# Kernel tuning notes

Hardware: AMD Instinct MI355X
Metric: run time of the kernel (lower is better)

The kernel has to match this reference:

```python
import jax, jax.numpy as jnp
import numpy as np

N, E = 50000, 800000
D_IN, D_H, D_OUT = 128, 128, 64


def _gcn_conv(h, src, dst, norm, b, n):
    # h already linearly transformed: aggregate norm-weighted messages to dst
    msg = h[src] * norm[:, None]                      # [E+N, d]
    out = jax.ops.segment_sum(msg, dst, num_segments=n)
    return out + b


def setup_inputs() -> dict:
    key = jax.random.key(0)
    ks = jax.random.split(key, 5)
    x = jax.random.normal(ks[0], (N, D_IN), jnp.float32)
    edge_index = jax.random.randint(ks[1], (2, E), 0, N, jnp.int32)
    s1 = 1.0 / np.sqrt(D_IN)
    s2 = 1.0 / np.sqrt(D_H)
    W1 = jax.random.uniform(ks[2], (D_IN, D_H), jnp.float32, -s1, s1)
    b1 = jnp.zeros((D_H,), jnp.float32)
    W2 = jax.random.uniform(ks[3], (D_H, D_OUT), jnp.float32, -s2, s2)
    b2 = jnp.zeros((D_OUT,), jnp.float32)
    return {"x": x, "edge_index": edge_index, "W1": W1, "b1": b1, "W2": W2, "b2": b2}


def reference(x, edge_index, W1, b1, W2, b2):
    n = x.shape[0]
    loops = jnp.arange(n, dtype=edge_index.dtype)
    src = jnp.concatenate([edge_index[0], loops])     # add self-loops
    dst = jnp.concatenate([edge_index[1], loops])
    # symmetric normalization D^{-1/2} (A+I) D^{-1/2}; deg is in-degree incl. self-loop
    deg = jax.ops.segment_sum(jnp.ones(dst.shape[0], x.dtype), dst, num_segments=n)
    dinv = jnp.where(deg > 0, jax.lax.rsqrt(deg), 0.0)
    norm = dinv[src] * dinv[dst]
    h = _gcn_conv(x @ W1, src, dst, norm, b1, n)
    h = jax.nn.relu(h)                                # dropout = identity (eval)
    out = _gcn_conv(h @ W2, src, dst, norm, b2, n)
    return out
```

## Files before the change

kernel.cpp:

```cpp
#include <hip/hip_runtime.h>

typedef __bf16 bf16x8 __attribute__((ext_vector_type(8)));
typedef __bf16 bf16x4 __attribute__((ext_vector_type(4)));
typedef float  f32x4  __attribute__((ext_vector_type(4)));
typedef unsigned long long u64;

constexpr int PAD       = 64;
constexpr int BIN_SHIFT = 9;
constexpr int CAP       = 12288;
constexpr int SUBS      = 4;
constexpr int NPS       = 128;
constexpr int STR       = 68;
constexpr int CUR_STR   = 16;
constexpr int EPB       = 2048;


__global__ void init_k(int* __restrict__ bincur, __bf16* __restrict__ h1zero,
                       __bf16* __restrict__ h3zero) {
  int t = threadIdx.x;
  for (int i = t; i < 128 * CUR_STR; i += 256) bincur[i] = 0;
  if (t < 128) h1zero[t] = (__bf16)0.f;
  if (t < 64)  h3zero[t] = (__bf16)0.f;
}


__global__ __launch_bounds__(256) void bin_fill_k(
    const int* __restrict__ src, const int* __restrict__ dst,
    int* __restrict__ bincur, u64* __restrict__ bin_data, int E, int n) {
  __shared__ u64 pairs[EPB];
  __shared__ int binof[EPB];
  __shared__ int hist[128], cur[128], sbase[128], gbase[128];

  const int t = threadIdx.x;
  const int NB = (n + ((1 << BIN_SHIFT) - 1)) >> BIN_SHIFT;

  if (t < 128) { hist[t] = 0; cur[t] = 0; }
  __syncthreads();

  int base_e = blockIdx.x * EPB + t * 8;
  int m = E - base_e;
  m = m < 0 ? 0 : (m > 8 ? 8 : m);

  int sa[8], da[8], ba[8];
  if (m == 8) {
    int4 s0 = *reinterpret_cast<const int4*>(src + base_e);
    int4 s1 = *reinterpret_cast<const int4*>(src + base_e + 4);
    int4 d0 = *reinterpret_cast<const int4*>(dst + base_e);
    int4 d1 = *reinterpret_cast<const int4*>(dst + base_e + 4);
    sa[0]=s0.x; sa[1]=s0.y; sa[2]=s0.z; sa[3]=s0.w;
    sa[4]=s1.x; sa[5]=s1.y; sa[6]=s1.z; sa[7]=s1.w;
    da[0]=d0.x; da[1]=d0.y; da[2]=d0.z; da[3]=d0.w;
    da[4]=d1.x; da[5]=d1.y; da[6]=d1.z; da[7]=d1.w;
  } else {
    for (int k = 0; k < m; ++k) { sa[k] = src[base_e + k]; da[k] = dst[base_e + k]; }
  }
  for (int k = 0; k < m; ++k) {
    ba[k] = da[k] >> BIN_SHIFT;
    atomicAdd(&hist[ba[k]], 1);
  }
  __syncthreads();

  if (t < 128) sbase[t] = hist[t];
  __syncthreads();
  for (int off = 1; off < 128; off <<= 1) {
    int u = (t >= off && t < 128) ? sbase[t - off] : 0;
    __syncthreads();
    if (t < 128) sbase[t] += u;
    __syncthreads();
  }
  if (t < NB && hist[t] > 0) gbase[t] = atomicAdd(&bincur[t * CUR_STR], hist[t]);
  if (t < 128) sbase[t] -= hist[t];
  __syncthreads();

  for (int k = 0; k < m; ++k) {
    int b = ba[k];
    int q = atomicAdd(&cur[b], 1);
    int slot = sbase[b] + q;
    pairs[slot] = ((u64)(unsigned)sa[k] << 32) | (unsigned)da[k];
    binof[slot] = b;
  }
  __syncthreads();

  int T = E - blockIdx.x * EPB;
  T = T > EPB ? EPB : T;
  for (int i = t; i < T; i += 256) {
    int b = binof[i];
    int pos = gbase[b] + (i - sbase[b]);
    if (pos < CAP) bin_data[(size_t)b * CAP + pos] = pairs[i];
  }
}


__global__ __launch_bounds__(256) void gemm1_k(const float* __restrict__ X,
                                               const float* __restrict__ W,
                                               __bf16* __restrict__ C, int n) {
  constexpr int K = 128, KP = 136, NC = 128, NT = 8, KC = 4;
  __shared__ __bf16 WT[NC * KP];

  const int t = threadIdx.x;
  for (int idx = t; idx < K * NC / 4; idx += 256) {
    int col = idx & 127;
    int k4  = idx >> 7;
    bf16x4 w;
    w[0] = (__bf16)W[(k4 * 4 + 0) * NC + col];
    w[1] = (__bf16)W[(k4 * 4 + 1) * NC + col];
    w[2] = (__bf16)W[(k4 * 4 + 2) * NC + col];
    w[3] = (__bf16)W[(k4 * 4 + 3) * NC + col];
    *reinterpret_cast<bf16x4*>(&WT[col * KP + k4 * 4]) = w;
  }
  __syncthreads();

  const int lane = t & 63;
  const int lr = lane & 15;
  const int lg = lane >> 4;

  bf16x8 bfrag[NT][KC];
#pragma unroll
  for (int nt = 0; nt < NT; ++nt)
#pragma unroll
    for (int kc = 0; kc < KC; ++kc)
      bfrag[nt][kc] = *reinterpret_cast<const bf16x8*>(
          &WT[(nt * 16 + lr) * KP + kc * 32 + lg * 8]);

  const int gw = blockIdx.x * 4 + (t >> 6);
  const int nw = gridDim.x * 4;
  const int mtiles = (n + 15) / 16;

  for (int mt = gw; mt < mtiles; mt += nw) {
    const int row  = mt * 16 + lr;
    const int crow = (row < n) ? row : (n - 1);

    bf16x8 afrag[KC];
#pragma unroll
    for (int kc = 0; kc < KC; ++kc) {
      const f32x4* p = reinterpret_cast<const f32x4*>(
          X + (size_t)crow * K + kc * 32 + lg * 8);
      f32x4 v0 = p[0], v1 = p[1];
      bf16x8 a;
      a[0] = (__bf16)v0[0]; a[1] = (__bf16)v0[1];
      a[2] = (__bf16)v0[2]; a[3] = (__bf16)v0[3];
      a[4] = (__bf16)v1[0]; a[5] = (__bf16)v1[1];
      a[6] = (__bf16)v1[2]; a[7] = (__bf16)v1[3];
      afrag[kc] = a;
    }

    f32x4 acc[NT];
#pragma unroll
    for (int nt = 0; nt < NT; ++nt) acc[nt] = (f32x4){0.f, 0.f, 0.f, 0.f};
#pragma unroll
    for (int kc = 0; kc < KC; ++kc)
#pragma unroll
      for (int nt = 0; nt < NT; ++nt)
        acc[nt] = __builtin_amdgcn_mfma_f32_16x16x32_bf16(afrag[kc], bfrag[nt][kc],
                                                          acc[nt], 0, 0, 0);

#pragma unroll
    for (int nt = 0; nt < NT; ++nt)
#pragma unroll
      for (int r = 0; r < 4; ++r) {
        int orow = mt * 16 + lg * 4 + r;
        if (orow < n) C[(size_t)orow * NC + nt * 16 + lr] = (__bf16)acc[nt][r];
      }
  }
}


__global__ __launch_bounds__(512) void csr_build_k(const int* __restrict__ bincur,
                                                   const u64* __restrict__ bin_data,
                                                   int* __restrict__ srcs_pad,
                                                   int* __restrict__ cnt,
                                                   float* __restrict__ dinv,
                                                   __bf16* __restrict__ h1b, int n) {
  __shared__ int rows[NPS * STR];
  __shared__ int lcnt[NPS];

  const int bin = blockIdx.x / SUBS;
  const int sub = blockIdx.x % SUBS;
  const int lo  = (bin << BIN_SHIFT) + sub * NPS;
  const int hi  = min(n, (bin + 1) << BIN_SHIFT);

  for (int i = threadIdx.x; i < NPS * STR; i += 512) rows[i] = n;
  for (int i = threadIdx.x; i < NPS; i += 512) lcnt[i] = 0;
  __syncthreads();

  int cntE = bincur[bin * CUR_STR];
  cntE = cntE < CAP ? cntE : CAP;
  const u64* bd = bin_data + (size_t)bin * CAP;

  for (int i = threadIdx.x; i < cntE; i += 512) {
    u64 p = bd[i];
    int d = (int)(p & 0xffffffffu);
    unsigned l = (unsigned)(d - lo);
    if (l < (unsigned)NPS) {
      int q = atomicAdd(&lcnt[l], 1);
      if (q < PAD) rows[l * STR + q] = (int)(p >> 32);
    }
  }
  __syncthreads();

  for (int i = threadIdx.x; i < NPS * (PAD / 4); i += 512) {
    int nl = i >> 4;
    int c4 = i & 15;
    int g = lo + nl;
    if (g < hi)
      *reinterpret_cast<int4*>(&srcs_pad[(size_t)g * PAD + c4 * 4]) =
          *reinterpret_cast<const int4*>(&rows[nl * STR + c4 * 4]);
  }
  for (int i = threadIdx.x; i < NPS; i += 512) {
    int g = lo + i;
    if (g < hi) {
      int c = lcnt[i];
      cnt[g] = c;
      dinv[g] = rsqrtf((float)(c + 1));
    }
  }
  bf16x8* h8 = reinterpret_cast<bf16x8*>(h1b);
  for (int i = threadIdx.x; i < NPS * 16; i += 512) {
    int nl = i >> 4;
    int c8 = i & 15;
    int g = lo + nl;
    if (g < hi) {
      float di = rsqrtf((float)(lcnt[nl] + 1));
      bf16x8 v = h8[(size_t)g * 16 + c8];
      bf16x8 o;
#pragma unroll
      for (int q = 0; q < 8; ++q) o[q] = (__bf16)((float)v[q] * di);
      h8[(size_t)g * 16 + c8] = o;
    }
  }
}


__global__ __launch_bounds__(256) void gather_gemm2_k(
    const __bf16* __restrict__ h1b, const int* __restrict__ cnt,
    const int* __restrict__ srcs_pad, const float* __restrict__ dinv,
    const float* __restrict__ b1, const float* __restrict__ W2,
    __bf16* __restrict__ h3b, int n) {
  constexpr int K  = 128;
  constexpr int KP = 136;
  constexpr int NT = 4;
  constexpr int KC = 4;

  __shared__ __bf16 W2T[64 * KP];
  __shared__ __bf16 aggT[64 * KP];

  const int t = threadIdx.x;

  for (int idx = t; idx < K * 64 / 4; idx += 256) {
    int col = idx & 63;
    int k4  = idx >> 6;
    bf16x4 w;
    w[0] = (__bf16)W2[(k4 * 4 + 0) * 64 + col];
    w[1] = (__bf16)W2[(k4 * 4 + 1) * 64 + col];
    w[2] = (__bf16)W2[(k4 * 4 + 2) * 64 + col];
    w[3] = (__bf16)W2[(k4 * 4 + 3) * 64 + col];
    *reinterpret_cast<bf16x4*>(&W2T[col * KP + k4 * 4]) = w;
  }

  const int base = blockIdx.x * 64;
  const bf16x8* h8 = reinterpret_cast<const bf16x8*>(h1b);
#pragma unroll
  for (int pass = 0; pass < 4; ++pass) {
    const int nl = pass * 16 + (t >> 4);
    const int d8 = t & 15;
    const int node = base + nl;
    bf16x8 ov;
    if (node < n) {
      int c = cnt[node];
      c = c < PAD ? c : PAD;
      const float di = dinv[node];
      const int* row = srcs_pad + (size_t)node * PAD;
      bf16x8 sv = h8[(size_t)node * 16 + d8];

      float acc[8];
#pragma unroll
      for (int q = 0; q < 8; ++q) acc[q] = 0.f;

      for (int j0 = 0; j0 < c; j0 += 8) {
        int4 a = *reinterpret_cast<const int4*>(row + j0);
        int4 b = *reinterpret_cast<const int4*>(row + j0 + 4);
        bf16x8 v0 = h8[(size_t)a.x * 16 + d8];
        bf16x8 v1 = h8[(size_t)a.y * 16 + d8];
        bf16x8 v2 = h8[(size_t)a.z * 16 + d8];
        bf16x8 v3 = h8[(size_t)a.w * 16 + d8];
        bf16x8 v4 = h8[(size_t)b.x * 16 + d8];
        bf16x8 v5 = h8[(size_t)b.y * 16 + d8];
        bf16x8 v6 = h8[(size_t)b.z * 16 + d8];
        bf16x8 v7 = h8[(size_t)b.w * 16 + d8];
#pragma unroll
        for (int q = 0; q < 8; ++q)
          acc[q] += ((float)v0[q] + (float)v1[q]) + ((float)v2[q] + (float)v3[q]) +
                    ((float)v4[q] + (float)v5[q]) + ((float)v6[q] + (float)v7[q]);
      }
#pragma unroll
      for (int q = 0; q < 8; ++q) {
        float val = (acc[q] + (float)sv[q]) * di + b1[d8 * 8 + q];
        ov[q] = (__bf16)fmaxf(val, 0.f);
      }
    } else {
#pragma unroll
      for (int q = 0; q < 8; ++q) ov[q] = (__bf16)0.f;
    }
    *reinterpret_cast<bf16x8*>(&aggT[nl * KP + d8 * 8]) = ov;
  }
  __syncthreads();

  const int lane = t & 63;
  const int lr = lane & 15;
  const int lg = lane >> 4;
  const int wv = t >> 6;

  bf16x8 bfrag[NT][KC];
#pragma unroll
  for (int nt = 0; nt < NT; ++nt)
#pragma unroll
    for (int kc = 0; kc < KC; ++kc)
      bfrag[nt][kc] = *reinterpret_cast<const bf16x8*>(
          &W2T[(nt * 16 + lr) * KP + kc * 32 + lg * 8]);

  bf16x8 afrag[KC];
#pragma unroll
  for (int kc = 0; kc < KC; ++kc)
    afrag[kc] = *reinterpret_cast<const bf16x8*>(
        &aggT[(wv * 16 + lr) * KP + kc * 32 + lg * 8]);

  f32x4 acc[NT];
#pragma unroll
  for (int nt = 0; nt < NT; ++nt) acc[nt] = (f32x4){0.f, 0.f, 0.f, 0.f};
#pragma unroll
  for (int kc = 0; kc < KC; ++kc)
#pragma unroll
    for (int nt = 0; nt < NT; ++nt)
      acc[nt] = __builtin_amdgcn_mfma_f32_16x16x32_bf16(afrag[kc], bfrag[nt][kc],
                                                        acc[nt], 0, 0, 0);

#pragma unroll
  for (int r = 0; r < 4; ++r) {
    int orow = base + wv * 16 + lg * 4 + r;
    if (orow < n) {
      float sc = dinv[orow];
#pragma unroll
      for (int nt = 0; nt < NT; ++nt)
        h3b[(size_t)orow * 64 + nt * 16 + lr] = (__bf16)(acc[nt][r] * sc);
    }
  }
}


template<int D, bool RELU_OUT, bool OUT_BF16>
__global__ __launch_bounds__(256) void gather_bf_k(const __bf16* __restrict__ h,
                                                   const int* __restrict__ cnt,
                                                   const int* __restrict__ srcs_pad,
                                                   const float* __restrict__ dinv,
                                                   const float* __restrict__ bias,
                                                   void* __restrict__ outv, int n) {
  constexpr int L = D / 8;
  int t = blockIdx.x * 256 + threadIdx.x;
  int node = t / L;
  int d8 = t % L;
  if (node >= n) return;

  int c = cnt[node];
  c = c < PAD ? c : PAD;
  const float di = dinv[node];
  const int* row = srcs_pad + (size_t)node * PAD;
  const bf16x8* h8 = reinterpret_cast<const bf16x8*>(h);
  bf16x8 sv = h8[(size_t)node * L + d8];

  float acc[8];
#pragma unroll
  for (int q = 0; q < 8; ++q) acc[q] = 0.f;

  for (int j0 = 0; j0 < c; j0 += 8) {
    int4 a = *reinterpret_cast<const int4*>(row + j0);
    int4 b = *reinterpret_cast<const int4*>(row + j0 + 4);
    bf16x8 v0 = h8[(size_t)a.x * L + d8];
    bf16x8 v1 = h8[(size_t)a.y * L + d8];
    bf16x8 v2 = h8[(size_t)a.z * L + d8];
    bf16x8 v3 = h8[(size_t)a.w * L + d8];
    bf16x8 v4 = h8[(size_t)b.x * L + d8];
    bf16x8 v5 = h8[(size_t)b.y * L + d8];
    bf16x8 v6 = h8[(size_t)b.z * L + d8];
    bf16x8 v7 = h8[(size_t)b.w * L + d8];
#pragma unroll
    for (int q = 0; q < 8; ++q)
      acc[q] += ((float)v0[q] + (float)v1[q]) + ((float)v2[q] + (float)v3[q]) +
                ((float)v4[q] + (float)v5[q]) + ((float)v6[q] + (float)v7[q]);
  }

  float o[8];
#pragma unroll
  for (int q = 0; q < 8; ++q) {
    float b = bias[d8 * 8 + q];
    float val = (acc[q] + (float)sv[q]) * di + b;
    o[q] = RELU_OUT ? fmaxf(val, 0.f) : val;
  }

  if (OUT_BF16) {
    bf16x8 ov;
#pragma unroll
    for (int q = 0; q < 8; ++q) ov[q] = (__bf16)o[q];
    reinterpret_cast<bf16x8*>(outv)[(size_t)node * L + d8] = ov;
  } else {
    f32x4 lo = {o[0], o[1], o[2], o[3]};
    f32x4 hi = {o[4], o[5], o[6], o[7]};
    f32x4* op = reinterpret_cast<f32x4*>((float*)outv + (size_t)node * D + d8 * 8);
    op[0] = lo;
    op[1] = hi;
  }
}


extern "C" void kernel_launch(void* const* d_in, const int* in_sizes, int n_in,
                              void* d_out, int out_size, void* d_ws, size_t ws_size,
                              hipStream_t stream) {
  const float* x  = (const float*)d_in[0];
  const int*   ei = (const int*)d_in[1];
  const float* W1 = (const float*)d_in[2];
  const float* b1 = (const float*)d_in[3];
  const float* W2 = (const float*)d_in[4];
  const float* b2 = (const float*)d_in[5];

  const int n = in_sizes[0] / 128;
  const int E = in_sizes[1] / 2;
  const int* src = ei;
  const int* dst = ei + E;
  float* out = (float*)d_out;

  const int NB = (n + ((1 << BIN_SHIFT) - 1)) >> BIN_SHIFT;

  int*   bincur   = (int*)d_ws;
  int*   cnt      = (int*)d_ws + 128 * CUR_STR;
  float* dinv     = (float*)d_ws + 128 * CUR_STR + n;
  int*   srcs_pad = (int*)d_ws + 128 * CUR_STR + 2 * n;
  size_t w = (size_t)128 * CUR_STR + 2 * n + (size_t)n * PAD;
  __bf16* h1b     = (__bf16*)((int*)d_ws + w);   w += (size_t)(n + 1) * 64;
  __bf16* scratch = (__bf16*)((int*)d_ws + w);   w += (size_t)n * 64;
  __bf16* h3b     = (__bf16*)((int*)d_ws + w);
  u64* bin_data = (u64*)scratch;

  init_k<<<1, 256, 0, stream>>>(bincur, h1b + (size_t)n * 128, h3b + (size_t)n * 64);

  const int fillB = (E + EPB - 1) / EPB;
  bin_fill_k<<<fillB, 256, 0, stream>>>(src, dst, bincur, bin_data, E, n);

  gemm1_k<<<256, 256, 0, stream>>>(x, W1, h1b, n);

  csr_build_k<<<NB * SUBS, 512, 0, stream>>>(bincur, bin_data, srcs_pad, cnt, dinv, h1b, n);

  gather_gemm2_k<<<(n + 63) / 64, 256, 0, stream>>>(
      h1b, cnt, srcs_pad, dinv, b1, W2, h3b, n);

  {
    long long t = (long long)n * 8;
    gather_bf_k<64, false, false><<<(int)((t + 255) / 256), 256, 0, stream>>>(
        h3b, cnt, srcs_pad, dinv, b2, out, n);
  }
}
```

Before: 104.0 us.

## Fuse edge binning with first GEMM and shrink bins to one CSR block each

Merges the edge-binning kernel and the X·W1 GEMM into a single launch, with the first blocks doing binning and the rest doing the GEMM, so the two independent stages run concurrently and one launch goes away. The bin granularity drops from 512 to 128 nodes. Each CSR-build block now reads only its own bin's edges instead of scanning a four-times-larger shared bin, which removes the redundant filtering. The costs are a 512-entry histogram and scan in the binning path, fewer GEMM blocks (128 instead of 256), and a smaller per-bin capacity of 3072 edges, which could overflow on skewed graphs.

```diff
diff --git a/kernel.cpp b/kernel.cpp
--- a/kernel.cpp
+++ b/kernel.cpp
@@ -6,9 +6,9 @@
 typedef unsigned long long u64;
 
 constexpr int PAD       = 64;
-constexpr int BIN_SHIFT = 9;
-constexpr int CAP       = 12288;
-constexpr int SUBS      = 4;
+constexpr int BIN_SHIFT = 7;
+constexpr int NBMAX     = 512;
+constexpr int CAP       = 3072;
 constexpr int NPS       = 128;
 constexpr int STR       = 68;
 constexpr int CUR_STR   = 16;
@@ -18,86 +18,97 @@
 __global__ void init_k(int* __restrict__ bincur, __bf16* __restrict__ h1zero,
                        __bf16* __restrict__ h3zero) {
   int t = threadIdx.x;
-  for (int i = t; i < 128 * CUR_STR; i += 256) bincur[i] = 0;
+  for (int i = t; i < NBMAX * CUR_STR; i += 256) bincur[i] = 0;
   if (t < 128) h1zero[t] = (__bf16)0.f;
   if (t < 64)  h3zero[t] = (__bf16)0.f;
 }
 
 
-__global__ __launch_bounds__(256) void bin_fill_k(
+__global__ __launch_bounds__(256) void fused_bin_gemm_k(
     const int* __restrict__ src, const int* __restrict__ dst,
-    int* __restrict__ bincur, u64* __restrict__ bin_data, int E, int n) {
-  __shared__ u64 pairs[EPB];
-  __shared__ int binof[EPB];
-  __shared__ int hist[128], cur[128], sbase[128], gbase[128];
+    int* __restrict__ bincur, u64* __restrict__ bin_data, int E, int fillB,
+    const float* __restrict__ X, const float* __restrict__ W,
+    __bf16* __restrict__ C, int n) {
+  constexpr int K = 128, KP = 136, NC = 128, NT = 8, KC = 4;
+
+  __shared__ __align__(16) char smem[NC * KP * 2];
 
   const int t = threadIdx.x;
-  const int NB = (n + ((1 << BIN_SHIFT) - 1)) >> BIN_SHIFT;
-
-  if (t < 128) { hist[t] = 0; cur[t] = 0; }
-  __syncthreads();
-
-  int base_e = blockIdx.x * EPB + t * 8;
-  int m = E - base_e;
-  m = m < 0 ? 0 : (m > 8 ? 8 : m);
-
-  int sa[8], da[8], ba[8];
-  if (m == 8) {
-    int4 s0 = *reinterpret_cast<const int4*>(src + base_e);
-    int4 s1 = *reinterpret_cast<const int4*>(src + base_e + 4);
-    int4 d0 = *reinterpret_cast<const int4*>(dst + base_e);
-    int4 d1 = *reinterpret_cast<const int4*>(dst + base_e + 4);
-    sa[0]=s0.x; sa[1]=s0.y; sa[2]=s0.z; sa[3]=s0.w;
-    sa[4]=s1.x; sa[5]=s1.y; sa[6]=s1.z; sa[7]=s1.w;
-    da[0]=d0.x; da[1]=d0.y; da[2]=d0.z; da[3]=d0.w;
-    da[4]=d1.x; da[5]=d1.y; da[6]=d1.z; da[7]=d1.w;
-  } else {
-    for (int k = 0; k < m; ++k) { sa[k] = src[base_e + k]; da[k] = dst[base_e + k]; }
-  }
-  for (int k = 0; k < m; ++k) {
-    ba[k] = da[k] >> BIN_SHIFT;
-    atomicAdd(&hist[ba[k]], 1);
-  }
-  __syncthreads();
-
-  if (t < 128) sbase[t] = hist[t];
-  __syncthreads();
-  for (int off = 1; off < 128; off <<= 1) {
-    int u = (t >= off && t < 128) ? sbase[t - off] : 0;
+
+  if ((int)blockIdx.x < fillB) {
+    u64* pairs = (u64*)smem;
+    int* binof = (int*)(smem + 16384);
+    int* hist  = (int*)(smem + 24576);
+    int* cur   = (int*)(smem + 26624);
+    int* sbase = (int*)(smem + 28672);
+    int* gbase = (int*)(smem + 30720);
+    int* p     = (int*)(smem + 32768);
+    const int NB = (n + ((1 << BIN_SHIFT) - 1)) >> BIN_SHIFT;
+
+    for (int i = t; i < NBMAX; i += 256) { hist[i] = 0; cur[i] = 0; }
     __syncthreads();
-    if (t < 128) sbase[t] += u;
+
+    int base_e = blockIdx.x * EPB + t * 8;
+    int m = E - base_e;
+    m = m < 0 ? 0 : (m > 8 ? 8 : m);
+
+    int sa[8], da[8], ba[8];
+    if (m == 8) {
+      int4 s0 = *reinterpret_cast<const int4*>(src + base_e);
+      int4 s1 = *reinterpret_cast<const int4*>(src + base_e + 4);
+      int4 d0 = *reinterpret_cast<const int4*>(dst + base_e);
+      int4 d1 = *reinterpret_cast<const int4*>(dst + base_e + 4);
+      sa[0]=s0.x; sa[1]=s0.y; sa[2]=s0.z; sa[3]=s0.w;
+      sa[4]=s1.x; sa[5]=s1.y; sa[6]=s1.z; sa[7]=s1.w;
+      da[0]=d0.x; da[1]=d0.y; da[2]=d0.z; da[3]=d0.w;
+      da[4]=d1.x; da[5]=d1.y; da[6]=d1.z; da[7]=d1.w;
+    } else {
+      for (int k = 0; k < m; ++k) { sa[k] = src[base_e + k]; da[k] = dst[base_e + k]; }
+    }
+    for (int k = 0; k < m; ++k) {
+      ba[k] = da[k] >> BIN_SHIFT;
+      atomicAdd(&hist[ba[k]], 1);
+    }
     __syncthreads();
-  }
-  if (t < NB && hist[t] > 0) gbase[t] = atomicAdd(&bincur[t * CUR_STR], hist[t]);
-  if (t < 128) sbase[t] -= hist[t];
-  __syncthreads();
-
-  for (int k = 0; k < m; ++k) {
-    int b = ba[k];
-    int q = atomicAdd(&cur[b], 1);
-    int slot = sbase[b] + q;
-    pairs[slot] = ((u64)(unsigned)sa[k] << 32) | (unsigned)da[k];
-    binof[slot] = b;
-  }
-  __syncthreads();
-
-  int T = E - blockIdx.x * EPB;
-  T = T > EPB ? EPB : T;
-  for (int i = t; i < T; i += 256) {
-    int b = binof[i];
-    int pos = gbase[b] + (i - sbase[b]);
-    if (pos < CAP) bin_data[(size_t)b * CAP + pos] = pairs[i];
-  }
-}
-
-
-__global__ __launch_bounds__(256) void gemm1_k(const float* __restrict__ X,
-                                               const float* __restrict__ W,
-                                               __bf16* __restrict__ C, int n) {
-  constexpr int K = 128, KP = 136, NC = 128, NT = 8, KC = 4;
-  __shared__ __bf16 WT[NC * KP];
-
-  const int t = threadIdx.x;
+
+    p[t] = hist[2 * t] + hist[2 * t + 1];
+    __syncthreads();
+    for (int off = 1; off < 256; off <<= 1) {
+      int u = (t >= off) ? p[t - off] : 0;
+      __syncthreads();
+      p[t] += u;
+      __syncthreads();
+    }
+    {
+      int ex = (t == 0) ? 0 : p[t - 1];
+      sbase[2 * t]     = ex;
+      sbase[2 * t + 1] = ex + hist[2 * t];
+    }
+    for (int b = t; b < NBMAX; b += 256)
+      if (b < NB && hist[b] > 0)
+        gbase[b] = atomicAdd(&bincur[b * CUR_STR], hist[b]);
+    __syncthreads();
+
+    for (int k = 0; k < m; ++k) {
+      int b = ba[k];
+      int q = atomicAdd(&cur[b], 1);
+      int slot = sbase[b] + q;
+      pairs[slot] = ((u64)(unsigned)sa[k] << 32) | (unsigned)da[k];
+      binof[slot] = b;
+    }
+    __syncthreads();
+
+    int T = E - blockIdx.x * EPB;
+    T = T > EPB ? EPB : T;
+    for (int i = t; i < T; i += 256) {
+      int b = binof[i];
+      int pos = gbase[b] + (i - sbase[b]);
+      if (pos < CAP) bin_data[(size_t)b * CAP + pos] = pairs[i];
+    }
+    return;
+  }
+
+  __bf16* WT = (__bf16*)smem;
   for (int idx = t; idx < K * NC / 4; idx += 256) {
     int col = idx & 127;
     int k4  = idx >> 7;
@@ -122,8 +133,8 @@
       bfrag[nt][kc] = *reinterpret_cast<const bf16x8*>(
           &WT[(nt * 16 + lr) * KP + kc * 32 + lg * 8]);
 
-  const int gw = blockIdx.x * 4 + (t >> 6);
-  const int nw = gridDim.x * 4;
+  const int gw = (blockIdx.x - fillB) * 4 + (t >> 6);
+  const int nw = (gridDim.x - fillB) * 4;
   const int mtiles = (n + 15) / 16;
 
   for (int mt = gw; mt < mtiles; mt += nw) {
@@ -133,9 +144,9 @@
     bf16x8 afrag[KC];
 #pragma unroll
     for (int kc = 0; kc < KC; ++kc) {
-      const f32x4* p = reinterpret_cast<const f32x4*>(
+      const f32x4* p4 = reinterpret_cast<const f32x4*>(
           X + (size_t)crow * K + kc * 32 + lg * 8);
-      f32x4 v0 = p[0], v1 = p[1];
+      f32x4 v0 = p4[0], v1 = p4[1];
       bf16x8 a;
       a[0] = (__bf16)v0[0]; a[1] = (__bf16)v0[1];
       a[2] = (__bf16)v0[2]; a[3] = (__bf16)v0[3];
@@ -174,10 +185,9 @@
   __shared__ int rows[NPS * STR];
   __shared__ int lcnt[NPS];
 
-  const int bin = blockIdx.x / SUBS;
-  const int sub = blockIdx.x % SUBS;
-  const int lo  = (bin << BIN_SHIFT) + sub * NPS;
-  const int hi  = min(n, (bin + 1) << BIN_SHIFT);
+  const int bin = blockIdx.x;
+  const int lo  = bin << BIN_SHIFT;
+  const int hi  = min(n, lo + NPS);
 
   for (int i = threadIdx.x; i < NPS * STR; i += 512) rows[i] = n;
   for (int i = threadIdx.x; i < NPS; i += 512) lcnt[i] = 0;
@@ -427,13 +437,13 @@
   const int* dst = ei + E;
   float* out = (float*)d_out;
 
-  const int NB = (n + ((1 << BIN_SHIFT) - 1)) >> BIN_SHIFT;
+  const int NBIN = (n + ((1 << BIN_SHIFT) - 1)) >> BIN_SHIFT;
 
   int*   bincur   = (int*)d_ws;
-  int*   cnt      = (int*)d_ws + 128 * CUR_STR;
-  float* dinv     = (float*)d_ws + 128 * CUR_STR + n;
-  int*   srcs_pad = (int*)d_ws + 128 * CUR_STR + 2 * n;
-  size_t w = (size_t)128 * CUR_STR + 2 * n + (size_t)n * PAD;
+  int*   cnt      = (int*)d_ws + NBMAX * CUR_STR;
+  float* dinv     = (float*)d_ws + NBMAX * CUR_STR + n;
+  int*   srcs_pad = (int*)d_ws + NBMAX * CUR_STR + 2 * n;
+  size_t w = (size_t)NBMAX * CUR_STR + 2 * n + (size_t)n * PAD;
   __bf16* h1b     = (__bf16*)((int*)d_ws + w);   w += (size_t)(n + 1) * 64;
   __bf16* scratch = (__bf16*)((int*)d_ws + w);   w += (size_t)n * 64;
   __bf16* h3b     = (__bf16*)((int*)d_ws + w);
@@ -442,11 +452,11 @@
   init_k<<<1, 256, 0, stream>>>(bincur, h1b + (size_t)n * 128, h3b + (size_t)n * 64);
 
   const int fillB = (E + EPB - 1) / EPB;
-  bin_fill_k<<<fillB, 256, 0, stream>>>(src, dst, bincur, bin_data, E, n);
-
-  gemm1_k<<<256, 256, 0, stream>>>(x, W1, h1b, n);
-
-  csr_build_k<<<NB * SUBS, 512, 0, stream>>>(bincur, bin_data, srcs_pad, cnt, dinv, h1b, n);
+  const int gemmB = 128;
+  fused_bin_gemm_k<<<fillB + gemmB, 256, 0, stream>>>(
+      src, dst, bincur, bin_data, E, fillB, x, W1, h1b, n);
+
+  csr_build_k<<<NBIN, 512, 0, stream>>>(bincur, bin_data, srcs_pad, cnt, dinv, h1b, n);
 
   gather_gemm2_k<<<(n + 63) / 64, 256, 0, stream>>>(
       h1b, cnt, srcs_pad, dinv, b1, W2, h3b, n);
```

Result: no change. 106.0 us (+2.0%).

## Halve bin width for CSR build and shrink gather_gemm2 node tile to 32

Applied to the files above, without the earlier changes.

Bins now cover 256 nodes instead of 512 (up to 256 bins), so each csr_build block scans only the edges of a bin half as large, roughly halving redundant bin reads per block. The bin_fill histogram and prefix scan grow to 256 entries. gather_gemm2 now processes 32 nodes per block and splits the MFMA output columns across wave pairs, doubling the block count to improve occupancy and latency hiding in the gather. The cost is more global atomics and scan work per bin_fill block, and each gather_gemm2 block reloading W2 for half as many nodes.

```diff
diff --git a/kernel.cpp b/kernel.cpp
--- a/kernel.cpp
+++ b/kernel.cpp
@@ -6,19 +6,21 @@
 typedef unsigned long long u64;
 
 constexpr int PAD       = 64;
-constexpr int BIN_SHIFT = 9;
-constexpr int CAP       = 12288;
-constexpr int SUBS      = 4;
+constexpr int BIN_SHIFT = 8;
+constexpr int NBMAX     = 256;
+constexpr int CAP       = 6144;
+constexpr int SUBS      = 2;
 constexpr int NPS       = 128;
 constexpr int STR       = 68;
 constexpr int CUR_STR   = 16;
 constexpr int EPB       = 2048;
+constexpr int GGN       = 32;
 
 
 __global__ void init_k(int* __restrict__ bincur, __bf16* __restrict__ h1zero,
                        __bf16* __restrict__ h3zero) {
   int t = threadIdx.x;
-  for (int i = t; i < 128 * CUR_STR; i += 256) bincur[i] = 0;
+  for (int i = t; i < NBMAX * CUR_STR; i += 256) bincur[i] = 0;
   if (t < 128) h1zero[t] = (__bf16)0.f;
   if (t < 64)  h3zero[t] = (__bf16)0.f;
 }
@@ -29,12 +31,12 @@
     int* __restrict__ bincur, u64* __restrict__ bin_data, int E, int n) {
   __shared__ u64 pairs[EPB];
   __shared__ int binof[EPB];
-  __shared__ int hist[128], cur[128], sbase[128], gbase[128];
+  __shared__ int hist[NBMAX], cur[NBMAX], sbase[NBMAX], gbase[NBMAX];
 
   const int t = threadIdx.x;
   const int NB = (n + ((1 << BIN_SHIFT) - 1)) >> BIN_SHIFT;
 
-  if (t < 128) { hist[t] = 0; cur[t] = 0; }
+  hist[t] = 0; cur[t] = 0;
   __syncthreads();
 
   int base_e = blockIdx.x * EPB + t * 8;
@@ -60,16 +62,16 @@
   }
   __syncthreads();
 
-  if (t < 128) sbase[t] = hist[t];
-  __syncthreads();
-  for (int off = 1; off < 128; off <<= 1) {
-    int u = (t >= off && t < 128) ? sbase[t - off] : 0;
+  sbase[t] = hist[t];
+  __syncthreads();
+  for (int off = 1; off < 256; off <<= 1) {
+    int u = (t >= off) ? sbase[t - off] : 0;
     __syncthreads();
-    if (t < 128) sbase[t] += u;
+    sbase[t] += u;
     __syncthreads();
   }
   if (t < NB && hist[t] > 0) gbase[t] = atomicAdd(&bincur[t * CUR_STR], hist[t]);
-  if (t < 128) sbase[t] -= hist[t];
+  sbase[t] -= hist[t];
   __syncthreads();
 
   for (int k = 0; k < m; ++k) {
@@ -177,7 +179,7 @@
   const int bin = blockIdx.x / SUBS;
   const int sub = blockIdx.x % SUBS;
   const int lo  = (bin << BIN_SHIFT) + sub * NPS;
-  const int hi  = min(n, (bin + 1) << BIN_SHIFT);
+  const int hi  = min(n, lo + NPS);
 
   for (int i = threadIdx.x; i < NPS * STR; i += 512) rows[i] = n;
   for (int i = threadIdx.x; i < NPS; i += 512) lcnt[i] = 0;
@@ -238,11 +240,10 @@
     __bf16* __restrict__ h3b, int n) {
   constexpr int K  = 128;
   constexpr int KP = 136;
-  constexpr int NT = 4;
   constexpr int KC = 4;
 
   __shared__ __bf16 W2T[64 * KP];
-  __shared__ __bf16 aggT[64 * KP];
+  __shared__ __bf16 aggT[GGN * KP];
 
   const int t = threadIdx.x;
 
@@ -257,10 +258,10 @@
     *reinterpret_cast<bf16x4*>(&W2T[col * KP + k4 * 4]) = w;
   }
 
-  const int base = blockIdx.x * 64;
+  const int base = blockIdx.x * GGN;
   const bf16x8* h8 = reinterpret_cast<const bf16x8*>(h1b);
 #pragma unroll
-  for (int pass = 0; pass < 4; ++pass) {
+  for (int pass = 0; pass < 2; ++pass) {
     const int nl = pass * 16 + (t >> 4);
     const int d8 = t & 15;
     const int node = base + nl;
@@ -309,39 +310,41 @@
   const int lr = lane & 15;
   const int lg = lane >> 4;
   const int wv = t >> 6;
-
-  bf16x8 bfrag[NT][KC];
-#pragma unroll
-  for (int nt = 0; nt < NT; ++nt)
+  const int mrow = (wv & 1) * 16;
+  const int ch   = wv >> 1;
+
+  bf16x8 bfrag[2][KC];
+#pragma unroll
+  for (int nt = 0; nt < 2; ++nt)
 #pragma unroll
     for (int kc = 0; kc < KC; ++kc)
       bfrag[nt][kc] = *reinterpret_cast<const bf16x8*>(
-          &W2T[(nt * 16 + lr) * KP + kc * 32 + lg * 8]);
+          &W2T[((ch * 2 + nt) * 16 + lr) * KP + kc * 32 + lg * 8]);
 
   bf16x8 afrag[KC];
 #pragma unroll
   for (int kc = 0; kc < KC; ++kc)
     afrag[kc] = *reinterpret_cast<const bf16x8*>(
-        &aggT[(wv * 16 + lr) * KP + kc * 32 + lg * 8]);
-
-  f32x4 acc[NT];
-#pragma unroll
-  for (int nt = 0; nt < NT; ++nt) acc[nt] = (f32x4){0.f, 0.f, 0.f, 0.f};
+        &aggT[(mrow + lr) * KP + kc * 32 + lg * 8]);
+
+  f32x4 acc[2];
+#pragma unroll
+  for (int nt = 0; nt < 2; ++nt) acc[nt] = (f32x4){0.f, 0.f, 0.f, 0.f};
 #pragma unroll
   for (int kc = 0; kc < KC; ++kc)
 #pragma unroll
-    for (int nt = 0; nt < NT; ++nt)
+    for (int nt = 0; nt < 2; ++nt)
       acc[nt] = __builtin_amdgcn_mfma_f32_16x16x32_bf16(afrag[kc], bfrag[nt][kc],
                                                         acc[nt], 0, 0, 0);
 
 #pragma unroll
   for (int r = 0; r < 4; ++r) {
-    int orow = base + wv * 16 + lg * 4 + r;
+    int orow = base + mrow + lg * 4 + r;
     if (orow < n) {
       float sc = dinv[orow];
 #pragma unroll
-      for (int nt = 0; nt < NT; ++nt)
-        h3b[(size_t)orow * 64 + nt * 16 + lr] = (__bf16)(acc[nt][r] * sc);
+      for (int nt = 0; nt < 2; ++nt)
+        h3b[(size_t)orow * 64 + (ch * 2 + nt) * 16 + lr] = (__bf16)(acc[nt][r] * sc);
     }
   }
 }
@@ -427,13 +430,13 @@
   const int* dst = ei + E;
   float* out = (float*)d_out;
 
-  const int NB = (n + ((1 << BIN_SHIFT) - 1)) >> BIN_SHIFT;
+  const int NBIN = (n + ((1 << BIN_SHIFT) - 1)) >> BIN_SHIFT;
 
   int*   bincur   = (int*)d_ws;
-  int*   cnt      = (int*)d_ws + 128 * CUR_STR;
-  float* dinv     = (float*)d_ws + 128 * CUR_STR + n;
-  int*   srcs_pad = (int*)d_ws + 128 * CUR_STR + 2 * n;
-  size_t w = (size_t)128 * CUR_STR + 2 * n + (size_t)n * PAD;
+  int*   cnt      = (int*)d_ws + NBMAX * CUR_STR;
+  float* dinv     = (float*)d_ws + NBMAX * CUR_STR + n;
+  int*   srcs_pad = (int*)d_ws + NBMAX * CUR_STR + 2 * n;
+  size_t w = (size_t)NBMAX * CUR_STR + 2 * n + (size_t)n * PAD;
   __bf16* h1b     = (__bf16*)((int*)d_ws + w);   w += (size_t)(n + 1) * 64;
   __bf16* scratch = (__bf16*)((int*)d_ws + w);   w += (size_t)n * 64;
   __bf16* h3b     = (__bf16*)((int*)d_ws + w);
@@ -446,9 +449,9 @@
 
   gemm1_k<<<256, 256, 0, stream>>>(x, W1, h1b, n);
 
-  csr_build_k<<<NB * SUBS, 512, 0, stream>>>(bincur, bin_data, srcs_pad, cnt, dinv, h1b, n);
-
-  gather_gemm2_k<<<(n + 63) / 64, 256, 0, stream>>>(
+  csr_build_k<<<NBIN * SUBS, 512, 0, stream>>>(bincur, bin_data, srcs_pad, cnt, dinv, h1b, n);
+
+  gather_gemm2_k<<<(n + GGN - 1) / GGN, 256, 0, stream>>>(
       h1b, cnt, srcs_pad, dinv, b1, W2, h3b, n);
 
   {
```

Measured after the change: 103.1 us. About the same (-0.9%).
